# Kernel tuning notes

Measured on AMD Instinct MI355X. Metric: run time of the kernel, lower is better.

Reference implementation:

```python
import jax, jax.numpy as jnp
import numpy as np

NEG_INF = -1.0e9  # matches torch masked_fill value

def setup_inputs() -> dict:
    key = jax.random.key(0)
    kq, kk, kv, km = jax.random.split(key, 4)
    B, S, D = 16, 2048, 128
    query = jax.random.normal(kq, (B, S, D), dtype=jnp.float32)
    k = jax.random.normal(kk, (B, S, D), dtype=jnp.float32)
    value = jax.random.normal(kv, (B, S, D), dtype=jnp.float32)
    mask = jax.random.randint(km, (B, S, S), 0, 2).astype(jnp.bool_)
    return {"query": query, "key": k, "value": value, "mask": mask}

def reference(query, key, value, mask):
    # scores: [B, Sq, Sk]
    D = key.shape[-1]
    scale = jnp.sqrt(jnp.asarray(D, dtype=query.dtype))
    scores = jnp.einsum('bqd,bkd->bqk', query, key) / scale
    scores = jnp.where(mask, jnp.asarray(NEG_INF, dtype=scores.dtype), scores)
    attn = jax.nn.softmax(scores, axis=2)
    # dropout p=0.0 -> identity in eval/reference
    out = jnp.einsum('bqk,bkd->bqd', attn, value)
    return out, attn
```

## Files before the change

### kernel.cpp

```cpp
#include <hip/hip_runtime.h>

#define S 2048
#define Dh 128
#define NB 16
#define OUT_ELEMS ((size_t)NB * S * Dh)
#define NEG_BIG -1.0e9f
#define SCALE 0.08838834764831845f

typedef __attribute__((ext_vector_type(8))) short bf16x8;
typedef __attribute__((ext_vector_type(4))) float f32x4;
typedef __attribute__((ext_vector_type(4))) short s16x4;

__device__ __forceinline__ short f2bf(float x) {
    unsigned u = __float_as_uint(x);
    u += 0x7fffu + ((u >> 16) & 1u);
    return (short)(u >> 16);
}

__device__ __forceinline__ s16x4 pack4(float4 v) {
    s16x4 r;
    r.x = f2bf(v.x); r.y = f2bf(v.y); r.z = f2bf(v.z); r.w = f2bf(v.w);
    return r;
}

__global__ void detect_mask(const unsigned char* __restrict__ m, int* __restrict__ flag) {
    __shared__ int any;
    if (threadIdx.x == 0) any = 0;
    __syncthreads();
    int t = threadIdx.x;
    unsigned char v = (unsigned char)(m[t * 4 + 1] | m[t * 4 + 2] | m[t * 4 + 3]);
    if (v) atomicOr(&any, 1);
    __syncthreads();
    if (t == 0) *flag = any;
}

__global__ __launch_bounds__(256) void transpose_v(const float* __restrict__ V,
                                                   short* __restrict__ Vt) {
    const int kb = blockIdx.x, b = blockIdx.y;
    const float* Vb = V + ((size_t)b * S + kb * 64) * Dh;
    short* VtB = Vt + (size_t)b * Dh * S;
    __shared__ float Ls[64][132];
    const int t = threadIdx.x;
#pragma unroll
    for (int i = 0; i < 8; i++) {
        int idx = t + i * 256;
        int r = idx >> 5, c = (idx & 31) << 2;
        *(float4*)&Ls[r][c] = *(const float4*)(Vb + r * Dh + c);
    }
    __syncthreads();
#pragma unroll
    for (int i = 0; i < 8; i++) {
        int idx = t + i * 256;
        int n = idx >> 4, kc = (idx & 15) << 2;
        s16x4 o;
        o.x = f2bf(Ls[kc + 0][n]);
        o.y = f2bf(Ls[kc + 1][n]);
        o.z = f2bf(Ls[kc + 2][n]);
        o.w = f2bf(Ls[kc + 3][n]);
        *(s16x4*)(VtB + (size_t)n * S + kb * 64 + kc) = o;
    }
}

__global__ __launch_bounds__(256, 2) void qk_kernel(const float* __restrict__ Q,
                                                    const float* __restrict__ Km,
                                                    float* __restrict__ Sc) {
    const int kt = blockIdx.x, qt = blockIdx.y, b = blockIdx.z;
    const float* Qb = Q + ((size_t)b * S + qt * 128) * Dh;
    const float* Kb = Km + ((size_t)b * S + kt * 128) * Dh;
    __shared__ short As[128][72];
    __shared__ short Bs[128][72];
    const int t = threadIdx.x;
    const int w = t >> 6, lane = t & 63, fr = lane & 15, quad = lane >> 4;
    const int mw = (w >> 1) * 64, nw = (w & 1) * 64;
    f32x4 acc[4][4] = {};

    for (int k0 = 0; k0 < Dh; k0 += 64) {
        __syncthreads();
#pragma unroll
        for (int i = 0; i < 8; i++) {
            int idx = t + i * 256;
            int r = idx >> 4, c = (idx & 15) << 2;
            float4 qv = *(const float4*)(Qb + r * Dh + k0 + c);
            float4 kv = *(const float4*)(Kb + r * Dh + k0 + c);
            *(s16x4*)&As[r][c] = pack4(qv);
            *(s16x4*)&Bs[r][c] = pack4(kv);
        }
        __syncthreads();
#pragma unroll
        for (int kc = 0; kc < 2; kc++) {
            const int ko = kc * 32 + quad * 8;
            bf16x8 af[4], bf[4];
#pragma unroll
            for (int mi = 0; mi < 4; mi++) af[mi] = *(const bf16x8*)&As[mw + mi * 16 + fr][ko];
#pragma unroll
            for (int ni = 0; ni < 4; ni++) bf[ni] = *(const bf16x8*)&Bs[nw + ni * 16 + fr][ko];
#pragma unroll
            for (int mi = 0; mi < 4; mi++)
#pragma unroll
                for (int ni = 0; ni < 4; ni++)
                    acc[mi][ni] = __builtin_amdgcn_mfma_f32_16x16x32_bf16(af[mi], bf[ni], acc[mi][ni], 0, 0, 0);
        }
    }

    float* ScB = Sc + (size_t)b * S * S;
#pragma unroll
    for (int mi = 0; mi < 4; mi++)
#pragma unroll
        for (int ni = 0; ni < 4; ni++)
#pragma unroll
            for (int r = 0; r < 4; r++) {
                int row = qt * 128 + mw + mi * 16 + quad * 4 + r;
                int col = kt * 128 + nw + ni * 16 + fr;
                ScB[(size_t)row * S + col] = acc[mi][ni][r] * SCALE;
            }
}

__global__ __launch_bounds__(256) void softmax_kernel(float* __restrict__ Sc,
                                                      const void* __restrict__ maskp,
                                                      const int* __restrict__ flagp) {
    const int b = blockIdx.y;
    const int w = threadIdx.x >> 6, lane = threadIdx.x & 63;
    const int row = blockIdx.x * 4 + w;
    float* R = Sc + ((size_t)b * S + row) * S;
    float4* R4 = (float4*)R;
    const int flag = flagp ? *flagp : 0;

    float sv[32];
    if (flag) {
        const uchar4* M4 = (const uchar4*)((const unsigned char*)maskp + ((size_t)b * S + row) * S);
#pragma unroll
        for (int j = 0; j < 8; j++) {
            float4 v = R4[lane + 64 * j];
            uchar4 m = M4[lane + 64 * j];
            sv[4 * j + 0] = m.x ? NEG_BIG : v.x;
            sv[4 * j + 1] = m.y ? NEG_BIG : v.y;
            sv[4 * j + 2] = m.z ? NEG_BIG : v.z;
            sv[4 * j + 3] = m.w ? NEG_BIG : v.w;
        }
    } else {
        const int4* M4 = (const int4*)((const int*)maskp + ((size_t)b * S + row) * S);
#pragma unroll
        for (int j = 0; j < 8; j++) {
            float4 v = R4[lane + 64 * j];
            int4 m = M4[lane + 64 * j];
            sv[4 * j + 0] = m.x ? NEG_BIG : v.x;
            sv[4 * j + 1] = m.y ? NEG_BIG : v.y;
            sv[4 * j + 2] = m.z ? NEG_BIG : v.z;
            sv[4 * j + 3] = m.w ? NEG_BIG : v.w;
        }
    }

    float mx = sv[0];
#pragma unroll
    for (int i = 1; i < 32; i++) mx = fmaxf(mx, sv[i]);
    for (int o = 32; o > 0; o >>= 1) mx = fmaxf(mx, __shfl_xor(mx, o, 64));

    float sum = 0.f;
#pragma unroll
    for (int i = 0; i < 32; i++) {
        sv[i] = __expf(sv[i] - mx);
        sum += sv[i];
    }
    for (int o = 32; o > 0; o >>= 1) sum += __shfl_xor(sum, o, 64);
    const float inv = 1.0f / sum;

#pragma unroll
    for (int j = 0; j < 8; j++) {
        float4 p;
        p.x = sv[4 * j + 0] * inv;
        p.y = sv[4 * j + 1] * inv;
        p.z = sv[4 * j + 2] * inv;
        p.w = sv[4 * j + 3] * inv;
        R4[lane + 64 * j] = p;
    }
}

__global__ __launch_bounds__(256, 2) void pv_kernel(const float* __restrict__ Sc,
                                                    const float* __restrict__ V,
                                                    const short* __restrict__ Vt,
                                                    const int useVt,
                                                    float* __restrict__ Out) {
    const int mt = blockIdx.x, b = blockIdx.y;
    const float* ScB = Sc + (size_t)b * S * S + (size_t)mt * 64 * S;
    const float* Vb = V + (size_t)b * S * Dh;
    const short* VtB = Vt + (size_t)b * Dh * S;
    float* OutB = Out + ((size_t)b * S + mt * 64) * Dh;
    __shared__ short As[64][72];
    const int t = threadIdx.x, w = t >> 6, lane = t & 63, fr = lane & 15, quad = lane >> 4;
    const int mw = (w >> 1) * 32, nw = (w & 1) * 64;
    f32x4 acc[2][4] = {};

    for (int k0 = 0; k0 < S; k0 += 64) {
        __syncthreads();
#pragma unroll
        for (int i = 0; i < 4; i++) {
            int idx = t + i * 256;
            int r = idx >> 4, c = (idx & 15) << 2;
            float4 v = *(const float4*)(ScB + (size_t)r * S + k0 + c);
            *(s16x4*)&As[r][c] = pack4(v);
        }
        __syncthreads();
#pragma unroll
        for (int kc = 0; kc < 2; kc++) {
            const int ko = kc * 32 + quad * 8;
            bf16x8 af[2], bf[4];
#pragma unroll
            for (int mi = 0; mi < 2; mi++) af[mi] = *(const bf16x8*)&As[mw + mi * 16 + fr][ko];
            if (useVt) {
#pragma unroll
                for (int ni = 0; ni < 4; ni++)
                    bf[ni] = *(const bf16x8*)(VtB + (size_t)(nw + ni * 16 + fr) * S + k0 + ko);
            } else {
#pragma unroll
                for (int ni = 0; ni < 4; ni++) {
                    int n = nw + ni * 16 + fr;
#pragma unroll
                    for (int j = 0; j < 8; j++) bf[ni][j] = f2bf(Vb[(size_t)(k0 + ko + j) * Dh + n]);
                }
            }
#pragma unroll
            for (int mi = 0; mi < 2; mi++)
#pragma unroll
                for (int ni = 0; ni < 4; ni++)
                    acc[mi][ni] = __builtin_amdgcn_mfma_f32_16x16x32_bf16(af[mi], bf[ni], acc[mi][ni], 0, 0, 0);
        }
    }

#pragma unroll
    for (int mi = 0; mi < 2; mi++)
#pragma unroll
        for (int ni = 0; ni < 4; ni++)
#pragma unroll
            for (int r = 0; r < 4; r++) {
                int row = mw + mi * 16 + quad * 4 + r;
                int col = nw + ni * 16 + fr;
                OutB[(size_t)row * Dh + col] = acc[mi][ni][r];
            }
}

extern "C" void kernel_launch(void* const* d_in, const int* in_sizes, int n_in,
                              void* d_out, int out_size, void* d_ws, size_t ws_size,
                              hipStream_t stream) {
    const float* Q = (const float*)d_in[0];
    const float* Km = (const float*)d_in[1];
    const float* V = (const float*)d_in[2];
    const void* M = d_in[3];
    float* out = (float*)d_out;
    float* attn = out + OUT_ELEMS;

    const size_t VT_BYTES = (size_t)NB * Dh * S * sizeof(short);
    const int useVt = (ws_size >= VT_BYTES + 64) ? 1 : 0;
    int* flag = nullptr;
    if (ws_size >= (size_t)(useVt ? VT_BYTES + 64 : 64))
        flag = (int*)((char*)d_ws + (useVt ? VT_BYTES : 0));

    if (flag) detect_mask<<<1, 256, 0, stream>>>((const unsigned char*)M, flag);
    if (useVt) transpose_v<<<dim3(32, NB), 256, 0, stream>>>(V, (short*)d_ws);
    qk_kernel<<<dim3(16, 16, NB), 256, 0, stream>>>(Q, Km, attn);
    softmax_kernel<<<dim3(512, NB), 256, 0, stream>>>(attn, M, flag);
    pv_kernel<<<dim3(32, NB), 256, 0, stream>>>(attn, V, (const short*)d_ws, useVt, out);
}
```

Before: 752.2 us.

## Fuse masking and partial softmax stats into QK, normalize in PV

Applies the mask and computes per-tile row max and sum inside the QK kernel, writing partial stats to scratch in the output buffer. A small reduce kernel combines them, and the PV kernel exponentiates and normalizes scores on load while writing the final attention back. This removes the separate softmax pass over the S×S score matrix (one read and one write), at the cost of an extra mask load in QK, extra exp work, and a tiny reduction kernel. It requires enough workspace for the Vt and stats buffers, and otherwise falls back to the old path.

```diff
diff --git a/kernel.cpp b/kernel.cpp
--- a/kernel.cpp
+++ b/kernel.cpp
@@ -63,16 +63,48 @@
 
 __global__ __launch_bounds__(256, 2) void qk_kernel(const float* __restrict__ Q,
                                                     const float* __restrict__ Km,
-                                                    float* __restrict__ Sc) {
+                                                    float* __restrict__ Sc,
+                                                    const void* __restrict__ maskp,
+                                                    const int* __restrict__ flagp,
+                                                    float2* __restrict__ part,
+                                                    const int fuse) {
     const int kt = blockIdx.x, qt = blockIdx.y, b = blockIdx.z;
     const float* Qb = Q + ((size_t)b * S + qt * 128) * Dh;
     const float* Kb = Km + ((size_t)b * S + kt * 128) * Dh;
     __shared__ short As[128][72];
     __shared__ short Bs[128][72];
+    __shared__ __align__(16) unsigned char Ms[128][144];
     const int t = threadIdx.x;
     const int w = t >> 6, lane = t & 63, fr = lane & 15, quad = lane >> 4;
     const int mw = (w >> 1) * 64, nw = (w & 1) * 64;
     f32x4 acc[4][4] = {};
+
+    if (fuse) {
+        const int flag = *flagp;
+        if (flag) {
+            const unsigned char* Mb = (const unsigned char*)maskp + ((size_t)b * S + qt * 128) * S + (size_t)kt * 128;
+#pragma unroll
+            for (int i = 0; i < 4; i++) {
+                int idx = t + i * 256;
+                int r = idx >> 3, c = (idx & 7) * 16;
+                *(int4*)&Ms[r][c] = *(const int4*)(Mb + (size_t)r * S + c);
+            }
+        } else {
+            const int* Mb = (const int*)maskp + ((size_t)b * S + qt * 128) * S + (size_t)kt * 128;
+#pragma unroll
+            for (int i = 0; i < 16; i++) {
+                int idx = t + i * 256;
+                int r = idx >> 5, c = (idx & 31) * 4;
+                int4 m = *(const int4*)(Mb + (size_t)r * S + c);
+                uchar4 o;
+                o.x = (unsigned char)(m.x != 0);
+                o.y = (unsigned char)(m.y != 0);
+                o.z = (unsigned char)(m.z != 0);
+                o.w = (unsigned char)(m.w != 0);
+                *(uchar4*)&Ms[r][c] = o;
+            }
+        }
+    }
 
     for (int k0 = 0; k0 < Dh; k0 += 64) {
         __syncthreads();
@@ -102,17 +134,62 @@
         }
     }
 
+    __syncthreads();
+    float2* pm = (float2*)&As[0][0];
     float* ScB = Sc + (size_t)b * S * S;
 #pragma unroll
     for (int mi = 0; mi < 4; mi++)
 #pragma unroll
-        for (int ni = 0; ni < 4; ni++)
-#pragma unroll
-            for (int r = 0; r < 4; r++) {
-                int row = qt * 128 + mw + mi * 16 + quad * 4 + r;
-                int col = kt * 128 + nw + ni * 16 + fr;
-                ScB[(size_t)row * S + col] = acc[mi][ni][r] * SCALE;
-            }
+        for (int r = 0; r < 4; r++) {
+            const int lrow = mw + mi * 16 + quad * 4 + r;
+            const size_t grow = (size_t)(qt * 128 + lrow);
+            float s[4];
+#pragma unroll
+            for (int ni = 0; ni < 4; ni++) {
+                const int lcol = nw + ni * 16 + fr;
+                float v = acc[mi][ni][r] * SCALE;
+                if (fuse && Ms[lrow][lcol]) v = NEG_BIG;
+                s[ni] = v;
+                ScB[grow * S + kt * 128 + lcol] = v;
+            }
+            if (fuse) {
+                float mx = fmaxf(fmaxf(s[0], s[1]), fmaxf(s[2], s[3]));
+#pragma unroll
+                for (int o = 8; o > 0; o >>= 1) mx = fmaxf(mx, __shfl_xor(mx, o, 64));
+                float l = __expf(s[0] - mx) + __expf(s[1] - mx) +
+                          __expf(s[2] - mx) + __expf(s[3] - mx);
+#pragma unroll
+                for (int o = 8; o > 0; o >>= 1) l += __shfl_xor(l, o, 64);
+                if (fr == 0) pm[lrow * 2 + (w & 1)] = make_float2(mx, l);
+            }
+        }
+
+    if (fuse) {
+        __syncthreads();
+        if (t < 128) {
+            float2 a = pm[t * 2 + 0], c = pm[t * 2 + 1];
+            float M = fmaxf(a.x, c.x);
+            float L = a.y * __expf(a.x - M) + c.y * __expf(c.x - M);
+            part[((size_t)(b * 16 + kt)) * S + qt * 128 + t] = make_float2(M, L);
+        }
+    }
+}
+
+__global__ __launch_bounds__(256) void reduce_stats(const float2* __restrict__ part,
+                                                    float2* __restrict__ stats) {
+    const int rid = blockIdx.x * 256 + threadIdx.x;
+    const int b = rid >> 11, row = rid & (S - 1);
+    float2 p[16];
+    float M = -3.4e38f;
+#pragma unroll
+    for (int kt = 0; kt < 16; kt++) {
+        p[kt] = part[((size_t)(b * 16 + kt)) * S + row];
+        M = fmaxf(M, p[kt].x);
+    }
+    float L = 0.f;
+#pragma unroll
+    for (int kt = 0; kt < 16; kt++) L += p[kt].y * __expf(p[kt].x - M);
+    stats[rid] = make_float2(M, 1.0f / L);
 }
 
 __global__ __launch_bounds__(256) void softmax_kernel(float* __restrict__ Sc,
@@ -175,20 +252,25 @@
     }
 }
 
-__global__ __launch_bounds__(256, 2) void pv_kernel(const float* __restrict__ Sc,
+__global__ __launch_bounds__(256, 2) void pv_kernel(float* __restrict__ Sc,
                                                     const float* __restrict__ V,
                                                     const short* __restrict__ Vt,
                                                     const int useVt,
-                                                    float* __restrict__ Out) {
+                                                    float* __restrict__ Out,
+                                                    const float2* __restrict__ stats,
+                                                    const int fuse) {
     const int mt = blockIdx.x, b = blockIdx.y;
-    const float* ScB = Sc + (size_t)b * S * S + (size_t)mt * 64 * S;
+    float* ScB = Sc + (size_t)b * S * S + (size_t)mt * 64 * S;
     const float* Vb = V + (size_t)b * S * Dh;
     const short* VtB = Vt + (size_t)b * Dh * S;
     float* OutB = Out + ((size_t)b * S + mt * 64) * Dh;
     __shared__ short As[64][72];
+    __shared__ float2 sstat[64];
     const int t = threadIdx.x, w = t >> 6, lane = t & 63, fr = lane & 15, quad = lane >> 4;
     const int mw = (w >> 1) * 32, nw = (w & 1) * 64;
     f32x4 acc[2][4] = {};
+
+    if (fuse && t < 64) sstat[t] = stats[(size_t)b * S + mt * 64 + t];
 
     for (int k0 = 0; k0 < S; k0 += 64) {
         __syncthreads();
@@ -197,6 +279,14 @@
             int idx = t + i * 256;
             int r = idx >> 4, c = (idx & 15) << 2;
             float4 v = *(const float4*)(ScB + (size_t)r * S + k0 + c);
+            if (fuse) {
+                float2 st = sstat[r];
+                v.x = __expf(v.x - st.x) * st.y;
+                v.y = __expf(v.y - st.x) * st.y;
+                v.z = __expf(v.z - st.x) * st.y;
+                v.w = __expf(v.w - st.x) * st.y;
+                *(float4*)(ScB + (size_t)r * S + k0 + c) = v;
+            }
             *(s16x4*)&As[r][c] = pack4(v);
         }
         __syncthreads();
@@ -249,14 +339,38 @@
     float* attn = out + OUT_ELEMS;
 
     const size_t VT_BYTES = (size_t)NB * Dh * S * sizeof(short);
-    const int useVt = (ws_size >= VT_BYTES + 64) ? 1 : 0;
+    const size_t STATS_BYTES = (size_t)NB * S * sizeof(float2);
+
+    int useVt = 0, fuse = 0;
+    short* Vt = nullptr;
+    float2* stats = nullptr;
     int* flag = nullptr;
-    if (ws_size >= (size_t)(useVt ? VT_BYTES + 64 : 64))
-        flag = (int*)((char*)d_ws + (useVt ? VT_BYTES : 0));
+
+    if (ws_size >= VT_BYTES + STATS_BYTES + 64) {
+        useVt = 1; fuse = 1;
+        Vt = (short*)d_ws;
+        stats = (float2*)((char*)d_ws + VT_BYTES);
+        flag = (int*)((char*)d_ws + VT_BYTES + STATS_BYTES);
+    } else if (ws_size >= VT_BYTES + 64) {
+        useVt = 1;
+        Vt = (short*)d_ws;
+        flag = (int*)((char*)d_ws + VT_BYTES);
+    } else if (ws_size >= 64) {
+        flag = (int*)d_ws;
+    }
+
+    float2* part = (float2*)d_out;
 
     if (flag) detect_mask<<<1, 256, 0, stream>>>((const unsigned char*)M, flag);
-    if (useVt) transpose_v<<<dim3(32, NB), 256, 0, stream>>>(V, (short*)d_ws);
-    qk_kernel<<<dim3(16, 16, NB), 256, 0, stream>>>(Q, Km, attn);
-    softmax_kernel<<<dim3(512, NB), 256, 0, stream>>>(attn, M, flag);
-    pv_kernel<<<dim3(32, NB), 256, 0, stream>>>(attn, V, (const short*)d_ws, useVt, out);
-}
+    if (useVt) transpose_v<<<dim3(32, NB), 256, 0, stream>>>(V, Vt);
+
+    qk_kernel<<<dim3(16, 16, NB), 256, 0, stream>>>(Q, Km, attn, M, flag, part, fuse);
+
+    if (fuse) {
+        reduce_stats<<<dim3((NB * S) / 256), 256, 0, stream>>>(part, stats);
+        pv_kernel<<<dim3(32, NB), 256, 0, stream>>>(attn, V, Vt, useVt, out, stats, 1);
+    } else {
+        softmax_kernel<<<dim3(512, NB), 256, 0, stream>>>(attn, M, flag);
+        pv_kernel<<<dim3(32, NB), 256, 0, stream>>>(attn, V, Vt, useVt, out, nullptr, 0);
+    }
+}
```

Result: no change. 762.9 us (+1.4%).
